# Kernel optimization log

Hardware: AMD Instinct MI355X
Metric: run time of the kernel (lower is better)

## Reference

```python
import jax, jax.numpy as jnp
import numpy as np

N, E = 50000, 400000
IN, H, D, K = 256, 128, 64, 8
BN_EPS = 1e-5


def _gcn(x, row, col, W, b, n):
    # PyG GCNConv: x' = D^{-1/2} (A + I) D^{-1/2} (x @ W) + b
    h = x @ W
    loop = jnp.arange(n)
    r = jnp.concatenate([row, loop])
    c = jnp.concatenate([col, loop])
    deg = jax.ops.segment_sum(jnp.ones_like(c, dtype=h.dtype), c, num_segments=n)
    dinv = jnp.where(deg > 0, jax.lax.rsqrt(deg), 0.0)
    norm = dinv[r] * dinv[c]                      # [E+N]
    out = jax.ops.segment_sum(h[r] * norm[:, None], c, num_segments=n)
    return out + b


def setup_inputs() -> dict:
    key = jax.random.key(0)
    ks = jax.random.split(key, 10)
    x = jax.random.normal(ks[0], (N, IN), dtype=jnp.float32)
    edge_index = jax.random.randint(ks[1], (2, E), 0, N)
    s = 0.05
    return {
        "x": x,
        "edge_index": edge_index,
        "gamma": jnp.ones((IN,), jnp.float32),
        "beta": jnp.zeros((IN,), jnp.float32),
        "W1": jax.random.normal(ks[2], (IN, H), jnp.float32) * s,
        "b1": jnp.zeros((H,), jnp.float32),
        "W2": jax.random.normal(ks[3], (H, D), jnp.float32) * s,
        "b2": jnp.zeros((D,), jnp.float32),
        "Wt": jax.random.normal(ks[4], (D, D, K), jnp.float32) * s,
        "V": jax.random.normal(ks[5], (K, 2 * D), jnp.float32) * s,
        "bt": jax.random.normal(ks[6], (K, 1), jnp.float32) * s,
        "U": jax.random.normal(ks[7], (1, K), jnp.float32) * s,
    }


def reference(x, edge_index, gamma, beta, W1, b1, W2, b2, Wt, V, bt, U):
    row, col = edge_index[0], edge_index[1]
    # BatchNorm1d (training-mode batch stats, biased variance)
    mean = jnp.mean(x, axis=0)
    var = jnp.mean((x - mean) ** 2, axis=0)
    xn = (x - mean) * jax.lax.rsqrt(var + BN_EPS) * gamma + beta
    # encode: GCN -> leaky_relu(0.1) -> GCN
    h = _gcn(xn, row, col, W1, b1, N)
    h = jnp.where(h >= 0, h, 0.1 * h)
    z = _gcn(h, row, col, W2, b2, N)                 # [N, D]
    # decode: per-edge NTN bilinear + linear + tanh + U + sigmoid
    src = z[row]                                      # [E, D]
    dst = z[col]                                      # [E, D]
    bil = jnp.einsum('ed,dck,ec->ek', src, Wt, dst)   # [E, K] batched bilinear
    lin = jnp.concatenate([src, dst], axis=-1) @ V.T  # [E, K]
    t = jnp.tanh(bil + lin + bt[:, 0][None, :])       # [E, K] (dropout: eval mode)
    logits = t @ U[0]                                 # [E]
    return jax.nn.sigmoid(logits)
```

## Files before the change

### kernel.cpp

```cpp
#include <hip/hip_runtime.h>

#define NNODE 50000
#define NEDGE 400000

#define OFF_SUMS    0x0000
#define OFF_SUMSQ   0x0400
#define OFF_SCALE   0x0800
#define OFF_SHIFT   0x0C00
#define OFF_CSHIFT  0x1000
#define OFF_PART    0x1400
#define OFF_BPREF   0x1600
#define OFF_W1P     0x2000
#define OFF_WT2     0x22000
#define OFF_DEG     0x42000
#define OFF_OFFS    0x73000
#define OFF_CURS    0xA4000
#define OFF_DINV    0xD5000
#define OFF_CSR     0x106000
#define OFF_CSRE    0x290000
#define OFF_LV      0x420000
#define OFF_H0      0x800000
#define OFF_Z0      OFF_H0
#define OFF_Z       (OFF_H0 + 0xD00000)
#define OFF_H1      0x2100000
#define OFF_Q       OFF_H1

static __device__ __forceinline__ unsigned short f32_to_bf16(float f) {
  unsigned int u = __float_as_uint(f);
  u += 0x7fffu + ((u >> 16) & 1u);
  return (unsigned short)(u >> 16);
}

__global__ __launch_bounds__(256) void bn_stats(const float* __restrict__ x,
                                                float* __restrict__ sums,
                                                float* __restrict__ sumsq) {
  const int t = threadIdx.x;
  const int per = (NNODE + gridDim.x - 1) / gridDim.x;
  const int r0 = blockIdx.x * per;
  const int r1 = min(NNODE, r0 + per);
  float s = 0.f, q = 0.f;
  for (int r = r0; r < r1; ++r) {
    float v = x[(size_t)r * 256 + t];
    s += v; q += v * v;
  }
  atomicAdd(&sums[t], s);
  atomicAdd(&sumsq[t], q);
}

__global__ void bn_finalize(const float* __restrict__ sums, const float* __restrict__ sumsq,
                            const float* __restrict__ gamma, const float* __restrict__ beta,
                            float* __restrict__ scale, float* __restrict__ shift) {
  const int i = threadIdx.x;
  float mean = sums[i] * (1.f / NNODE);
  float var  = sumsq[i] * (1.f / NNODE) - mean * mean;
  float sc   = rsqrtf(var + 1e-5f) * gamma[i];
  scale[i] = sc;
  shift[i] = beta[i] - mean * sc;
}

__global__ void make_w1p(const float* __restrict__ W1, const float* __restrict__ scale,
                         float* __restrict__ W1p) {
  const int idx = blockIdx.x * 256 + threadIdx.x;
  W1p[idx] = scale[idx >> 7] * W1[idx];
}

__global__ void make_cshift(const float* __restrict__ W1, const float* __restrict__ shift,
                            float* __restrict__ cshift) {
  const int j = threadIdx.x;
  float s = 0.f;
  for (int i = 0; i < 256; ++i) s += shift[i] * W1[i * 128 + j];
  cshift[j] = s;
}

__global__ void make_wt2(const float* __restrict__ Wt, float* __restrict__ Wt2) {
  const int idx = blockIdx.x * 256 + threadIdx.x;
  const int d = idx >> 9, ck = idx & 511;
  const int c = ck >> 3, k = ck & 7;
  Wt2[c * 512 + d * 8 + k] = Wt[idx];
}

__global__ __launch_bounds__(256) void count_deg(const int* __restrict__ col, int* __restrict__ deg) {
  const int e = blockIdx.x * 256 + threadIdx.x;
  if (e < NEDGE) atomicAdd(&deg[col[e]], 1);
}

__global__ __launch_bounds__(1024) void scan_a(const int* __restrict__ deg, int* __restrict__ offs,
                                               int* __restrict__ partials, float* __restrict__ dinv) {
  __shared__ int buf[1024];
  const int t = threadIdx.x;
  const int i = blockIdx.x * 1024 + t;
  const int v = (i < NNODE) ? deg[i] : 0;
  buf[t] = v;
  __syncthreads();
  for (int off = 1; off < 1024; off <<= 1) {
    int a = (t >= off) ? buf[t - off] : 0;
    __syncthreads();
    buf[t] += a;
    __syncthreads();
  }
  if (i < NNODE) {
    offs[i] = buf[t] - v;
    dinv[i] = rsqrtf((float)(v + 1));
  }
  if (t == 1023) partials[blockIdx.x] = buf[t];
}

__global__ void scan_b(const int* __restrict__ partials, int* __restrict__ bpref,
                       int* __restrict__ offs) {
  if (threadIdx.x == 0) {
    int run = 0;
    for (int b = 0; b < 49; ++b) { bpref[b] = run; run += partials[b]; }
    offs[NNODE] = run;
  }
}

__global__ __launch_bounds__(1024) void scan_c(int* __restrict__ offs, const int* __restrict__ bpref,
                                               int* __restrict__ cursor) {
  const int i = blockIdx.x * 1024 + threadIdx.x;
  if (i < NNODE) {
    int o = offs[i] + bpref[blockIdx.x];
    offs[i] = o;
    cursor[i] = o;
  }
}

__global__ __launch_bounds__(256) void fill_csr(const int* __restrict__ row, const int* __restrict__ col,
                                                int* __restrict__ cursor, int* __restrict__ csr_src,
                                                int* __restrict__ csr_eid) {
  const int e = blockIdx.x * 256 + threadIdx.x;
  if (e < NEDGE) {
    int c = col[e];
    int p = atomicAdd(&cursor[c], 1);
    csr_src[p] = row[e];
    csr_eid[p] = e;
  }
}

template <int BM, int BN, int BK, int TM, int TN, bool BF16OUT>
__global__ __launch_bounds__(256) void gemm_tiled(const float* __restrict__ A,
                                                  const float* __restrict__ B,
                                                  void* __restrict__ Cout,
                                                  const float* __restrict__ bias,
                                                  const float* __restrict__ rowscale,
                                                  int M, int Kd, int Nd) {
  constexpr int TX = BN / TN;
  constexpr int TY = BM / TM;
  constexpr int THREADS = TX * TY;
  __shared__ __align__(16) float As[BM][BK + 4];
  __shared__ __align__(16) float Bs[BK][BN];
  const int tid = threadIdx.x;
  const int tx = tid % TX, ty = tid / TX;
  const int m0 = blockIdx.x * BM, n0 = blockIdx.y * BN;

  float acc[TM][TN];
  for (int i = 0; i < TM; ++i)
    for (int j = 0; j < TN; ++j) acc[i][j] = 0.f;

  for (int k0 = 0; k0 < Kd; k0 += BK) {
    for (int i = tid; i < (BM * BK) / 4; i += THREADS) {
      int mm = i / (BK / 4), kq = i % (BK / 4);
      int gm = m0 + mm;
      float4 v = make_float4(0.f, 0.f, 0.f, 0.f);
      if (gm < M) v = *(const float4*)(A + (size_t)gm * Kd + k0 + kq * 4);
      *(float4*)(&As[mm][kq * 4]) = v;
    }
    for (int i = tid; i < (BK * BN) / 4; i += THREADS) {
      int kk = i / (BN / 4), nq = i % (BN / 4);
      *(float4*)(&Bs[kk][nq * 4]) = *(const float4*)(B + (size_t)(k0 + kk) * Nd + n0 + nq * 4);
    }
    __syncthreads();
#pragma unroll
    for (int kk = 0; kk < BK; ++kk) {
      float a[TM], b[TN];
#pragma unroll
      for (int i = 0; i < TM; ++i) a[i] = As[ty * TM + i][kk];
#pragma unroll
      for (int j4 = 0; j4 < TN / 4; ++j4) {
        float4 bv = *(const float4*)(&Bs[kk][tx * TN + j4 * 4]);
        b[j4 * 4 + 0] = bv.x; b[j4 * 4 + 1] = bv.y; b[j4 * 4 + 2] = bv.z; b[j4 * 4 + 3] = bv.w;
      }
#pragma unroll
      for (int i = 0; i < TM; ++i)
#pragma unroll
        for (int j = 0; j < TN; ++j) acc[i][j] = fmaf(a[i], b[j], acc[i][j]);
    }
    __syncthreads();
  }

  float bv[TN];
#pragma unroll
  for (int j = 0; j < TN; ++j) bv[j] = bias ? bias[n0 + tx * TN + j] : 0.f;

#pragma unroll
  for (int i = 0; i < TM; ++i) {
    int gm = m0 + ty * TM + i;
    if (gm >= M) continue;
    const float rs = rowscale ? rowscale[gm] : 1.f;
    if constexpr (BF16OUT) {
      unsigned short* C = (unsigned short*)Cout;
      alignas(16) unsigned short tmp[TN];
#pragma unroll
      for (int j = 0; j < TN; ++j) tmp[j] = f32_to_bf16((acc[i][j] + bv[j]) * rs);
      if constexpr (TN == 8) {
        *(uint4*)(C + (size_t)gm * Nd + n0 + tx * TN) = *(const uint4*)tmp;
      } else {
#pragma unroll
        for (int j = 0; j < TN; ++j) C[(size_t)gm * Nd + n0 + tx * TN + j] = tmp[j];
      }
    } else {
      float* C = (float*)Cout;
#pragma unroll
      for (int j4 = 0; j4 < TN / 4; ++j4) {
        float4 v;
        v.x = (acc[i][j4 * 4 + 0] + bv[j4 * 4 + 0]) * rs;
        v.y = (acc[i][j4 * 4 + 1] + bv[j4 * 4 + 1]) * rs;
        v.z = (acc[i][j4 * 4 + 2] + bv[j4 * 4 + 2]) * rs;
        v.w = (acc[i][j4 * 4 + 3] + bv[j4 * 4 + 3]) * rs;
        *(float4*)(C + (size_t)gm * Nd + n0 + tx * TN + j4 * 4) = v;
      }
    }
  }
}

template <int F, bool LEAKY>
__global__ __launch_bounds__(256) void agg_kernel(const float* __restrict__ hs,
                                                  const int* __restrict__ csr_src,
                                                  const int* __restrict__ offs,
                                                  const float* __restrict__ dinv,
                                                  const float* __restrict__ bias,
                                                  float* __restrict__ out) {
  constexpr int NPB = 256 / F;
  const int vth = blockIdx.x * NPB + threadIdx.x / F;
  const int v = __builtin_amdgcn_readfirstlane(vth);
  const int f = threadIdx.x % F;
  const float dv = dinv[v];
  const int j0 = offs[v], j1 = offs[v + 1];

  float a0 = hs[(size_t)v * F + f];
  float a1 = 0.f, a2 = 0.f, a3 = 0.f;

  for (int jb = j0; jb < j1; jb += 4) {
    const int jm = j1 - 1;
    const int r0 = csr_src[jb];
    const int r1 = csr_src[min(jb + 1, jm)];
    const int r2 = csr_src[min(jb + 2, jm)];
    const int r3 = csr_src[min(jb + 3, jm)];
    const float w1 = (jb + 1 <= jm) ? 1.f : 0.f;
    const float w2 = (jb + 2 <= jm) ? 1.f : 0.f;
    const float w3 = (jb + 3 <= jm) ? 1.f : 0.f;
    a0 += hs[(size_t)r0 * F + f];
    a1 = fmaf(w1, hs[(size_t)r1 * F + f], a1);
    a2 = fmaf(w2, hs[(size_t)r2 * F + f], a2);
    a3 = fmaf(w3, hs[(size_t)r3 * F + f], a3);
  }

  float o = ((a0 + a1) + (a2 + a3)) * dv + bias[f];
  if (LEAKY) o = (o >= 0.f) ? o : 0.1f * o;
  out[(size_t)v * F + f] = o;
}

__global__ __launch_bounds__(256) void lv_kernel(const float* __restrict__ z,
                                                 const float* __restrict__ V,
                                                 float* __restrict__ LV) {
  const int idx = blockIdx.x * 256 + threadIdx.x;
  if (idx >= NNODE * 16) return;
  const int v = idx >> 4, kk = idx & 15;
  const float* vr = V + (kk & 7) * 128 + ((kk & 8) ? 64 : 0);
  const float* zr = z + (size_t)v * 64;
  float s = 0.f;
#pragma unroll
  for (int d4 = 0; d4 < 16; ++d4) {
    float4 zv = *(const float4*)(zr + d4 * 4);
    float4 vv = *(const float4*)(vr + d4 * 4);
    s += zv.x * vv.x + zv.y * vv.y + zv.z * vv.z + zv.w * vv.w;
  }
  LV[idx] = s;
}

__global__ __launch_bounds__(256) void decode_kernel(const int* __restrict__ csr_src,
                                                     const int* __restrict__ csr_eid,
                                                     const int* __restrict__ offs,
                                                     const float* __restrict__ z,
                                                     const unsigned short* __restrict__ Q,
                                                     const float* __restrict__ LV,
                                                     const float* __restrict__ bt,
                                                     const float* __restrict__ U,
                                                     float* __restrict__ out) {
  __shared__ float qs[4][512];
  const int w = threadIdx.x >> 6, lane = threadIdx.x & 63;
  const int v = blockIdx.x * 4 + w;

  {
    const unsigned short* qrow = Q + (size_t)v * 512;
    union { uint4 r; unsigned short u[8]; } uu;
    uu.r = *(const uint4*)(qrow + lane * 8);
#pragma unroll
    for (int j = 0; j < 8; ++j)
      qs[w][lane * 8 + j] = __uint_as_float(((unsigned int)uu.u[j]) << 16);
  }
  __syncthreads();

  const int g = lane >> 3, k = lane & 7;
  const float uk = U[k];
  const float lvc = LV[(size_t)v * 16 + 8 + k] + bt[k];
  const int j0 = offs[v], j1 = offs[v + 1];

  for (int jb = j0; jb < j1; jb += 8) {
    const int j = jb + g;
    const bool act = (j < j1);
    const int r = act ? csr_src[j] : 0;
    const int eid = act ? csr_eid[j] : 0;
    const float4* zr = (const float4*)(z + (size_t)r * 64);
    float acc = 0.f;
#pragma unroll
    for (int d4 = 0; d4 < 16; ++d4) {
      float4 zv = zr[d4];
      const float* qp = &qs[w][d4 * 32 + k];
      acc = fmaf(zv.x, qp[0], acc);
      acc = fmaf(zv.y, qp[8], acc);
      acc = fmaf(zv.z, qp[16], acc);
      acc = fmaf(zv.w, qp[24], acc);
    }
    acc += LV[(size_t)r * 16 + k] + lvc;
    float c = tanhf(acc) * uk;
    c += __shfl_xor(c, 1);
    c += __shfl_xor(c, 2);
    c += __shfl_xor(c, 4);
    if (act && k == 0) out[eid] = 1.f / (1.f + __expf(-c));
  }
}

extern "C" void kernel_launch(void* const* d_in, const int* in_sizes, int n_in,
                              void* d_out, int out_size, void* d_ws, size_t ws_size,
                              hipStream_t stream) {
  const float* x     = (const float*)d_in[0];
  const int*   ei    = (const int*)d_in[1];
  const float* gamma = (const float*)d_in[2];
  const float* beta  = (const float*)d_in[3];
  const float* W1    = (const float*)d_in[4];
  const float* b1    = (const float*)d_in[5];
  const float* W2    = (const float*)d_in[6];
  const float* b2    = (const float*)d_in[7];
  const float* Wt    = (const float*)d_in[8];
  const float* V     = (const float*)d_in[9];
  const float* bt    = (const float*)d_in[10];
  const float* U     = (const float*)d_in[11];
  float* out = (float*)d_out;
  char* ws = (char*)d_ws;

  const int* row = ei;
  const int* col = ei + NEDGE;

  float* sums   = (float*)(ws + OFF_SUMS);
  float* sumsq  = (float*)(ws + OFF_SUMSQ);
  float* scale  = (float*)(ws + OFF_SCALE);
  float* shiftv = (float*)(ws + OFF_SHIFT);
  float* cshift = (float*)(ws + OFF_CSHIFT);
  int*   part   = (int*)(ws + OFF_PART);
  int*   bpref  = (int*)(ws + OFF_BPREF);
  float* W1p    = (float*)(ws + OFF_W1P);
  float* Wt2    = (float*)(ws + OFF_WT2);
  int*   deg    = (int*)(ws + OFF_DEG);
  int*   offs   = (int*)(ws + OFF_OFFS);
  int*   curs   = (int*)(ws + OFF_CURS);
  float* dinv   = (float*)(ws + OFF_DINV);
  int*   csr    = (int*)(ws + OFF_CSR);
  int*   csre   = (int*)(ws + OFF_CSRE);
  float* LV     = (float*)(ws + OFF_LV);
  float* h0     = (float*)(ws + OFF_H0);
  float* h1     = (float*)(ws + OFF_H1);
  float* z0     = (float*)(ws + OFF_Z0);
  float* zz     = (float*)(ws + OFF_Z);
  unsigned short* Q = (unsigned short*)(ws + OFF_Q);

  hipMemsetAsync(ws + OFF_SUMS, 0, 0x800, stream);
  hipMemsetAsync(ws + OFF_DEG, 0, NNODE * 4, stream);

  bn_stats<<<256, 256, 0, stream>>>(x, sums, sumsq);
  count_deg<<<1563, 256, 0, stream>>>(col, deg);
  bn_finalize<<<1, 256, 0, stream>>>(sums, sumsq, gamma, beta, scale, shiftv);
  make_w1p<<<128, 256, 0, stream>>>(W1, scale, W1p);
  make_cshift<<<1, 128, 0, stream>>>(W1, shiftv, cshift);
  make_wt2<<<128, 256, 0, stream>>>(Wt, Wt2);

  scan_a<<<49, 1024, 0, stream>>>(deg, offs, part, dinv);
  scan_b<<<1, 64, 0, stream>>>(part, bpref, offs);
  scan_c<<<49, 1024, 0, stream>>>(offs, bpref, curs);
  fill_csr<<<1563, 256, 0, stream>>>(row, col, curs, csr, csre);

  gemm_tiled<64, 128, 32, 4, 8, false><<<dim3(782, 1), 256, 0, stream>>>(x, W1p, h0, cshift, dinv, NNODE, 256, 128);
  agg_kernel<128, true><<<25000, 256, 0, stream>>>(h0, csr, offs, dinv, b1, h1);
  gemm_tiled<64, 64, 32, 4, 4, false><<<dim3(782, 1), 256, 0, stream>>>(h1, W2, z0, nullptr, dinv, NNODE, 128, 64);
  agg_kernel<64, false><<<12500, 256, 0, stream>>>(z0, csr, offs, dinv, b2, zz);

  gemm_tiled<64, 128, 32, 4, 8, true><<<dim3(782, 4), 256, 0, stream>>>(zz, Wt2, Q, nullptr, nullptr, NNODE, 64, 512);
  lv_kernel<<<3125, 256, 0, stream>>>(zz, V, LV);

  decode_kernel<<<12500, 256, 0, stream>>>(csr, csre, offs, zz, Q, LV, bt, U, out);
}
```

Before: 530.6 us.

## Split BatchNorm stats into two-pass partial reduction with vectorized loads

Replaces the single-pass column-statistics kernel, which has 256 blocks each walking about 196 rows one scalar per thread and then doing atomic adds, with two kernels. The first runs 1024 blocks that read rows as float4 and reduce across four wavefronts in shared memory, writing per-block partial sums to a scratch buffer. The second reduces those partials per column and writes the totals directly, so the memset and the atomics are no longer needed. The aim is more parallelism and wider loads over the 51 MB input. The cost is one extra launch and a scratch buffer that aliases h0, which is safe only because h0 is written later.

Result: faster. 464.5 us (-12.5%).

```diff
diff --git a/kernel.cpp b/kernel.cpp
--- a/kernel.cpp
+++ b/kernel.cpp
@@ -20,31 +20,74 @@
 #define OFF_CSRE    0x290000
 #define OFF_LV      0x420000
 #define OFF_H0      0x800000
+#define OFF_BNP     OFF_H0
 #define OFF_Z0      OFF_H0
 #define OFF_Z       (OFF_H0 + 0xD00000)
 #define OFF_H1      0x2100000
 #define OFF_Q       OFF_H1
 
+#define BN_NB 1024
+
 static __device__ __forceinline__ unsigned short f32_to_bf16(float f) {
   unsigned int u = __float_as_uint(f);
   u += 0x7fffu + ((u >> 16) & 1u);
   return (unsigned short)(u >> 16);
 }
 
-__global__ __launch_bounds__(256) void bn_stats(const float* __restrict__ x,
-                                                float* __restrict__ sums,
-                                                float* __restrict__ sumsq) {
-  const int t = threadIdx.x;
-  const int per = (NNODE + gridDim.x - 1) / gridDim.x;
-  const int r0 = blockIdx.x * per;
-  const int r1 = min(NNODE, r0 + per);
-  float s = 0.f, q = 0.f;
-  for (int r = r0; r < r1; ++r) {
-    float v = x[(size_t)r * 256 + t];
-    s += v; q += v * v;
-  }
-  atomicAdd(&sums[t], s);
-  atomicAdd(&sumsq[t], q);
+__global__ __launch_bounds__(256) void bn_stats1(const float* __restrict__ x,
+                                                 float* __restrict__ P) {
+  __shared__ float4 ls[4][64];
+  __shared__ float4 lq[4][64];
+  const int b = blockIdx.x, t = threadIdx.x;
+  const int w = t >> 6, l = t & 63;
+  const int rows = (NNODE + BN_NB - 1) / BN_NB;
+  const int r0 = b * rows;
+  const int r1 = min(NNODE, r0 + rows);
+  float4 s = make_float4(0.f, 0.f, 0.f, 0.f);
+  float4 q = make_float4(0.f, 0.f, 0.f, 0.f);
+  for (int r = r0 + w; r < r1; r += 4) {
+    float4 v = *(const float4*)(x + (size_t)r * 256 + l * 4);
+    s.x += v.x; s.y += v.y; s.z += v.z; s.w += v.w;
+    q.x = fmaf(v.x, v.x, q.x); q.y = fmaf(v.y, v.y, q.y);
+    q.z = fmaf(v.z, v.z, q.z); q.w = fmaf(v.w, v.w, q.w);
+  }
+  ls[w][l] = s; lq[w][l] = q;
+  __syncthreads();
+  if (t < 64) {
+    float4 s0 = ls[0][t], s1 = ls[1][t], s2 = ls[2][t], s3 = ls[3][t];
+    float4 q0 = lq[0][t], q1 = lq[1][t], q2 = lq[2][t], q3 = lq[3][t];
+    float4 ss = make_float4((s0.x + s1.x) + (s2.x + s3.x), (s0.y + s1.y) + (s2.y + s3.y),
+                            (s0.z + s1.z) + (s2.z + s3.z), (s0.w + s1.w) + (s2.w + s3.w));
+    float4 qq = make_float4((q0.x + q1.x) + (q2.x + q3.x), (q0.y + q1.y) + (q2.y + q3.y),
+                            (q0.z + q1.z) + (q2.z + q3.z), (q0.w + q1.w) + (q2.w + q3.w));
+    *(float4*)(P + (size_t)b * 512 + t * 4)       = ss;
+    *(float4*)(P + (size_t)b * 512 + 256 + t * 4) = qq;
+  }
+}
+
+__global__ __launch_bounds__(256) void bn_stats2(const float* __restrict__ P,
+                                                 float* __restrict__ sums,
+                                                 float* __restrict__ sumsq) {
+  __shared__ float red[256];
+  const int c = blockIdx.x, t = threadIdx.x;
+  float s = 0.f;
+  for (int i = t; i < BN_NB; i += 256) s += P[(size_t)i * 512 + c];
+  red[t] = s;
+  __syncthreads();
+  if (t < 128) red[t] += red[t + 128];
+  __syncthreads();
+  if (t < 64) {
+    float v = red[t] + red[t + 64];
+    v += __shfl_down(v, 32);
+    v += __shfl_down(v, 16);
+    v += __shfl_down(v, 8);
+    v += __shfl_down(v, 4);
+    v += __shfl_down(v, 2);
+    v += __shfl_down(v, 1);
+    if (t == 0) {
+      if (c < 256) sums[c] = v; else sumsq[c - 256] = v;
+    }
+  }
 }
 
 __global__ void bn_finalize(const float* __restrict__ sums, const float* __restrict__ sumsq,
@@ -367,17 +410,18 @@
   int*   csr    = (int*)(ws + OFF_CSR);
   int*   csre   = (int*)(ws + OFF_CSRE);
   float* LV     = (float*)(ws + OFF_LV);
+  float* bnp    = (float*)(ws + OFF_BNP);
   float* h0     = (float*)(ws + OFF_H0);
   float* h1     = (float*)(ws + OFF_H1);
   float* z0     = (float*)(ws + OFF_Z0);
   float* zz     = (float*)(ws + OFF_Z);
   unsigned short* Q = (unsigned short*)(ws + OFF_Q);
 
-  hipMemsetAsync(ws + OFF_SUMS, 0, 0x800, stream);
   hipMemsetAsync(ws + OFF_DEG, 0, NNODE * 4, stream);
 
-  bn_stats<<<256, 256, 0, stream>>>(x, sums, sumsq);
+  bn_stats1<<<BN_NB, 256, 0, stream>>>(x, bnp);
   count_deg<<<1563, 256, 0, stream>>>(col, deg);
+  bn_stats2<<<512, 256, 0, stream>>>(bnp, sums, sumsq);
   bn_finalize<<<1, 256, 0, stream>>>(sums, sumsq, gamma, beta, scale, shiftv);
   make_w1p<<<128, 256, 0, stream>>>(W1, scale, W1p);
   make_cshift<<<1, 128, 0, stream>>>(W1, shiftv, cshift);
```
